# Kernel optimization log

Measured on AMD Instinct MI355X. Metric: run time of the kernel, lower is better.

## Reference

```python
import jax, jax.numpy as jnp
import numpy as np

B, N, DIM = 4, 2048, 512
H, DH, ORDER, TOPK = 8, 64, 3, 64
INNER = H * DH
SCALE = DH ** -0.5


def setup_inputs() -> dict:
    key = jax.random.key(0)
    ks = jax.random.split(key, 6)
    x = jax.random.normal(ks[0], (B, N, DIM), dtype=jnp.float32)
    Wqkv = jax.random.normal(ks[1], (DIM, 3 * INNER), dtype=jnp.float32) * (DIM ** -0.5)
    bqkv = jax.random.normal(ks[2], (3 * INNER,), dtype=jnp.float32) * 0.01
    Wout = jax.random.normal(ks[3], (INNER, DIM), dtype=jnp.float32) * (INNER ** -0.5)
    bout = jax.random.normal(ks[4], (DIM,), dtype=jnp.float32) * 0.01
    # init per reset_parameters for non-softmax/sigmoid/tanh act: ones/order
    alphas_raw = jnp.ones((ORDER, H), dtype=jnp.float32) / ORDER
    return {"x": x, "Wqkv": Wqkv, "bqkv": bqkv, "Wout": Wout, "bout": bout, "alphas_raw": alphas_raw}


def reference(x, Wqkv, bqkv, Wout, bout, alphas_raw):
    b, n, _ = x.shape
    qkv = x @ Wqkv + bqkv                                   # (b, n, 3*inner)
    q, k, v = jnp.split(qkv, 3, axis=-1)
    to_heads = lambda t: t.reshape(b, n, H, DH).transpose(0, 2, 1, 3)  # (b, h, n, d)
    q, k, v = to_heads(q), to_heads(k), to_heads(v)
    scores = jnp.einsum('bhnd,bhmd->bhnm', q, k) * SCALE    # (b, h, n, n)
    # top-k masking along last dim (keep ties with k-th value)
    top_val = jax.lax.top_k(scores, TOPK)[0][..., -1:]
    scores = jnp.where(scores < top_val, -jnp.inf, scores)
    attn = jax.nn.softmax(scores, axis=-1)
    # fp32 polynomial filter (monomial basis)
    attn32 = attn.astype(jnp.float32)
    v_curr = v.astype(jnp.float32)
    alphas = jax.nn.gelu(alphas_raw.astype(jnp.float32), approximate=False)  # (order, h)
    res = jnp.zeros_like(v_curr)
    for i in range(ORDER):
        v_curr = attn32 @ v_curr
        res = res + alphas[i].reshape(1, H, 1, 1) * v_curr
    out = res.astype(x.dtype).transpose(0, 2, 1, 3).reshape(b, n, INNER)
    return out @ Wout + bout
```

## Files before the change

### kernel.cpp

```cpp
#include <hip/hip_runtime.h>
#include <hip/hip_bf16.h>

#define SLOTS 80

typedef __bf16 bf16x8 __attribute__((ext_vector_type(8)));
typedef float  f32x4  __attribute__((ext_vector_type(4)));
typedef unsigned short u16x8 __attribute__((ext_vector_type(8)));

__global__ __launch_bounds__(256)
void sgemm_bias(const float* __restrict__ A, const float* __restrict__ Bm,
                const float* __restrict__ bias, float* __restrict__ C,
                int M, int N, int K)
{
    __shared__ float As[16][132];
    __shared__ float Bs[16][132];

    const int t  = threadIdx.x;
    const int tx = t & 15, ty = t >> 4;
    const int bm = blockIdx.y << 7, bn = blockIdx.x << 7;

    const int arow = t >> 2,  ak4 = (t & 3) << 2;
    const int bkr  = t >> 5,  bc4 = (t & 31) << 2;

    float4 pa[2], pb[2];
#pragma unroll
    for (int s = 0; s < 2; ++s) {
        pa[s] = *(const float4*)&A[(size_t)(bm + arow + (s << 6)) * K + ak4];
        pb[s] = *(const float4*)&Bm[(size_t)(bkr + (s << 3)) * N + bn + bc4];
    }

    float acc[8][8] = {};

    for (int k0 = 0; k0 < K; k0 += 16) {
        __syncthreads();
#pragma unroll
        for (int s = 0; s < 2; ++s) {
            const int ar = arow + (s << 6);
            As[ak4 + 0][ar] = pa[s].x;
            As[ak4 + 1][ar] = pa[s].y;
            As[ak4 + 2][ar] = pa[s].z;
            As[ak4 + 3][ar] = pa[s].w;
            *(float4*)&Bs[bkr + (s << 3)][bc4] = pb[s];
        }
        __syncthreads();
        if (k0 + 16 < K) {
#pragma unroll
            for (int s = 0; s < 2; ++s) {
                pa[s] = *(const float4*)&A[(size_t)(bm + arow + (s << 6)) * K + k0 + 16 + ak4];
                pb[s] = *(const float4*)&Bm[(size_t)(k0 + 16 + bkr + (s << 3)) * N + bn + bc4];
            }
        }
#pragma unroll
        for (int kk = 0; kk < 16; ++kk) {
            float4 a0 = *(const float4*)&As[kk][(ty << 3) + 0];
            float4 a1 = *(const float4*)&As[kk][(ty << 3) + 4];
            float4 b0 = *(const float4*)&Bs[kk][(tx << 2)];
            float4 b1 = *(const float4*)&Bs[kk][64 + (tx << 2)];
            float ar[8] = {a0.x, a0.y, a0.z, a0.w, a1.x, a1.y, a1.z, a1.w};
            float br[8] = {b0.x, b0.y, b0.z, b0.w, b1.x, b1.y, b1.z, b1.w};
#pragma unroll
            for (int i = 0; i < 8; ++i)
#pragma unroll
                for (int j = 0; j < 8; ++j)
                    acc[i][j] = fmaf(ar[i], br[j], acc[i][j]);
        }
    }

    float bb[8];
#pragma unroll
    for (int j = 0; j < 4; ++j) {
        bb[j]     = bias[bn + (tx << 2) + j];
        bb[j + 4] = bias[bn + 64 + (tx << 2) + j];
    }
#pragma unroll
    for (int i = 0; i < 8; ++i) {
        const size_t row = (size_t)(bm + (ty << 3) + i);
        float4 o0 = {acc[i][0] + bb[0], acc[i][1] + bb[1], acc[i][2] + bb[2], acc[i][3] + bb[3]};
        float4 o1 = {acc[i][4] + bb[4], acc[i][5] + bb[5], acc[i][6] + bb[6], acc[i][7] + bb[7]};
        *(float4*)&C[row * N + bn + (tx << 2)]      = o0;
        *(float4*)&C[row * N + bn + 64 + (tx << 2)] = o1;
    }
}

__global__ __launch_bounds__(256)
void qk_split(const float* __restrict__ qkv, unsigned short* __restrict__ qfrag,
              unsigned short* __restrict__ kfrag)
{
    const int gid = blockIdx.x * 256 + threadIdx.x;
    const int dg = gid & 7;
    const int h  = (gid >> 3) & 7;
    const int n  = (gid >> 6) & 2047;
    const int b  = gid >> 17;
    const int bh = (b << 3) + h;

    const size_t src = ((size_t)(b * 2048 + n)) * 1536 + (h << 6) + (dg << 3);

    const int tb = n >> 4;
    const int c  = n & 15;
    const int ks = dg >> 2;
    const int ln = c | ((dg & 3) << 4);
    const size_t base0 = ((((size_t)bh * 128 + tb) * 6 + ks) * 64 + ln) * 8;

#pragma unroll
    for (int qk = 0; qk < 2; ++qk) {
        const float4 x0 = *(const float4*)&qkv[src + (qk ? 512 : 0)];
        const float4 x1 = *(const float4*)&qkv[src + (qk ? 512 : 0) + 4];
        unsigned short* outp = qk ? kfrag : qfrag;
        const float xs[8] = {x0.x, x0.y, x0.z, x0.w, x1.x, x1.y, x1.z, x1.w};
        u16x8 vh, vm, vl;
#pragma unroll
        for (int j = 0; j < 8; ++j) {
            const float x = xs[j];
            __hip_bfloat16 h0 = __float2bfloat16(x);
            const float f0 = __bfloat162float(h0);
            const float r1 = x - f0;
            __hip_bfloat16 h1 = __float2bfloat16(r1);
            const float f1 = __bfloat162float(h1);
            const float r2 = r1 - f1;
            __hip_bfloat16 h2 = __float2bfloat16(r2);
            vh[j] = *(unsigned short*)&h0;
            vm[j] = *(unsigned short*)&h1;
            vl[j] = *(unsigned short*)&h2;
        }
        *(u16x8*)(outp + base0)        = vh;
        *(u16x8*)(outp + base0 + 1024) = vm;
        *(u16x8*)(outp + base0 + 2048) = vl;
    }
}

__global__ __launch_bounds__(512, 2)
void scores_topk(const unsigned short* __restrict__ qfrag,
                 const unsigned short* __restrict__ kfrag,
                 float* __restrict__ svals,
                 unsigned short* __restrict__ sidx, int* __restrict__ scnt)
{
    __shared__ float S[16][2052];

    const int t    = threadIdx.x;
    const int lane = t & 63;
    const int wid  = t >> 6;
    const int id   = blockIdx.x;
    const int bh   = ((id >> 10) << 3) | (id & 7);
    const int rowblk = (id >> 3) & 127;
    const int r0   = rowblk << 4;

    const bf16x8* qf = (const bf16x8*)qfrag
                     + (((size_t)bh * 128 + rowblk) * 6) * 64 + lane;
    bf16x8 afr[6];
#pragma unroll
    for (int f = 0; f < 6; ++f) afr[f] = qf[f * 64];

    const bf16x8* kf = (const bf16x8*)kfrag + ((size_t)bh * 128 * 6) * 64 + lane;

#define MCHAIN(ACC, B0, B1, B2, B3, B4, B5)                                    \
        ACC = __builtin_amdgcn_mfma_f32_16x16x32_bf16(afr[0], B0, ACC, 0, 0, 0); \
        ACC = __builtin_amdgcn_mfma_f32_16x16x32_bf16(afr[1], B1, ACC, 0, 0, 0); \
        ACC = __builtin_amdgcn_mfma_f32_16x16x32_bf16(afr[0], B2, ACC, 0, 0, 0); \
        ACC = __builtin_amdgcn_mfma_f32_16x16x32_bf16(afr[1], B3, ACC, 0, 0, 0); \
        ACC = __builtin_amdgcn_mfma_f32_16x16x32_bf16(afr[2], B0, ACC, 0, 0, 0); \
        ACC = __builtin_amdgcn_mfma_f32_16x16x32_bf16(afr[3], B1, ACC, 0, 0, 0); \
        ACC = __builtin_amdgcn_mfma_f32_16x16x32_bf16(afr[2], B2, ACC, 0, 0, 0); \
        ACC = __builtin_amdgcn_mfma_f32_16x16x32_bf16(afr[3], B3, ACC, 0, 0, 0); \
        ACC = __builtin_amdgcn_mfma_f32_16x16x32_bf16(afr[0], B4, ACC, 0, 0, 0); \
        ACC = __builtin_amdgcn_mfma_f32_16x16x32_bf16(afr[1], B5, ACC, 0, 0, 0); \
        ACC = __builtin_amdgcn_mfma_f32_16x16x32_bf16(afr[4], B0, ACC, 0, 0, 0); \
        ACC = __builtin_amdgcn_mfma_f32_16x16x32_bf16(afr[5], B1, ACC, 0, 0, 0);

#define STEP2(I)                                                               \
    {                                                                          \
        const int ct0 = (((I) << 1) << 3) + wid;                               \
        const int ct1 = ((((I) << 1) | 1) << 3) + wid;                         \
        const bf16x8* kb0 = kf + (size_t)ct0 * 384;                            \
        const bf16x8* kb1 = kf + (size_t)ct1 * 384;                            \
        bf16x8 b0 = kb0[0];   bf16x8 b1 = kb0[64];  bf16x8 b2 = kb0[128];      \
        bf16x8 b3 = kb0[192]; bf16x8 b4 = kb0[256]; bf16x8 b5 = kb0[320];      \
        bf16x8 c0 = kb1[0];   bf16x8 c1 = kb1[64];  bf16x8 c2 = kb1[128];      \
        bf16x8 c3 = kb1[192]; bf16x8 c4 = kb1[256]; bf16x8 c5 = kb1[320];      \
        f32x4 acc0 = {0.f, 0.f, 0.f, 0.f};                                     \
        MCHAIN(acc0, b0, b1, b2, b3, b4, b5)                                   \
        f32x4 acc1 = {0.f, 0.f, 0.f, 0.f};                                     \
        MCHAIN(acc1, c0, c1, c2, c3, c4, c5)                                   \
        const int rbase = (lane >> 4) << 2;                                    \
        const int col0  = (ct0 << 4) + (lane & 15);                            \
        const int col1  = (ct1 << 4) + (lane & 15);                            \
        S[rbase + 0][col0] = acc0[0] * 0.125f;                                 \
        S[rbase + 1][col0] = acc0[1] * 0.125f;                                 \
        S[rbase + 2][col0] = acc0[2] * 0.125f;                                 \
        S[rbase + 3][col0] = acc0[3] * 0.125f;                                 \
        S[rbase + 0][col1] = acc1[0] * 0.125f;                                 \
        S[rbase + 1][col1] = acc1[1] * 0.125f;                                 \
        S[rbase + 2][col1] = acc1[2] * 0.125f;                                 \
        S[rbase + 3][col1] = acc1[3] * 0.125f;                                 \
    }

    STEP2(0) STEP2(1) STEP2(2) STEP2(3)
    STEP2(4) STEP2(5) STEP2(6) STEP2(7)
#undef STEP2
#undef MCHAIN

    __syncthreads();

    const unsigned long long pre64 = (1ull << lane) - 1ull;

#define PHASEB(RQ)                                                             \
    {                                                                          \
        const int rr = (wid << 1) + (RQ);                                      \
        float    fv[32];                                                       \
        unsigned uv[32];                                                       \
        _Pragma("unroll")                                                      \
        for (int m = 0; m < 32; ++m) {                                         \
            const float x = S[rr][lane + (m << 6)];                            \
            fv[m] = x;                                                         \
            const unsigned bx = __float_as_uint(x);                            \
            uv[m] = bx ^ (unsigned)(((int)bx >> 31) | 0x80000000);             \
        }                                                                      \
        unsigned lo = 0;                                                       \
        _Pragma("unroll 1")                                                    \
        for (int bit = 31; bit >= 0; --bit) {                                  \
            const unsigned mid = lo | (1u << bit);                             \
            int c = 0;                                                         \
            _Pragma("unroll")                                                  \
            for (int m = 0; m < 32; ++m)                                       \
                c += __popcll(__ballot(uv[m] >= mid));                         \
            if (c >= 64) {                                                     \
                lo = mid;                                                      \
                if (c == 64) break;                                            \
            }                                                                  \
        }                                                                      \
        unsigned um = 0;                                                       \
        _Pragma("unroll")                                                      \
        for (int m = 0; m < 32; ++m) um = uv[m] > um ? uv[m] : um;             \
        _Pragma("unroll")                                                      \
        for (int off = 1; off < 64; off <<= 1) {                               \
            const unsigned o = (unsigned)__shfl_xor((int)um, off, 64);         \
            um = o > um ? o : um;                                              \
        }                                                                      \
        const unsigned mbm = (um & 0x80000000u) ? (um ^ 0x80000000u) : ~um;    \
        const float Mx = __uint_as_float(mbm);                                 \
        float zs = 0.f;                                                        \
        _Pragma("unroll")                                                      \
        for (int m = 0; m < 32; ++m) {                                         \
            const bool keep = uv[m] >= lo;                                     \
            const float ex = keep ? __expf(fv[m] - Mx) : 0.f;                  \
            fv[m] = ex;                                                        \
            zs += ex;                                                          \
        }                                                                      \
        _Pragma("unroll")                                                      \
        for (int off = 1; off < 64; off <<= 1) zs += __shfl_xor(zs, off, 64);  \
        const float zinv = 1.0f / zs;                                          \
        const size_t grow = (size_t)bh * 2048 + r0 + rr;                       \
        float* vd           = svals + grow * SLOTS;                            \
        unsigned short* idp = sidx  + grow * SLOTS;                            \
        int base = 0;                                                          \
        _Pragma("unroll")                                                      \
        for (int m = 0; m < 32; ++m) {                                         \
            const bool keep = uv[m] >= lo;                                     \
            unsigned long long ball = __ballot(keep);                          \
            if (keep) {                                                        \
                const int my = base + __popcll(ball & pre64);                  \
                if (my < SLOTS) {                                              \
                    vd[my]  = fv[m] * zinv;                                    \
                    idp[my] = (unsigned short)(lane + (m << 6));               \
                }                                                              \
            }                                                                  \
            base += __popcll(ball);                                            \
        }                                                                      \
        if (lane == 0) scnt[grow] = base < SLOTS ? base : SLOTS;               \
    }

    PHASEB(0)
    PHASEB(1)
#undef PHASEB
}

__global__ __launch_bounds__(256)
void spmm(const float* __restrict__ svals, const unsigned short* __restrict__ sidx,
          const int* __restrict__ scnt, const float* __restrict__ qkv,
          const float* __restrict__ vin, float* __restrict__ vout,
          float* __restrict__ res, const float* __restrict__ alphas_raw, int order)
{
    const int lane = threadIdx.x & 63;
    const int id   = blockIdx.x;
    const int bh   = ((id & 7) << 2) | (id >> 12);
    const int nblk = (id >> 3) & 511;
    const int n    = (nblk << 2) + (threadIdx.x >> 6);
    const int gr   = (bh << 11) + n;
    const int b    = bh >> 3,  h = bh & 7;

    const float* vb;
    int stride;
    if (order == 0) { vb = qkv + (size_t)b * 2048 * 1536 + 1024 + (h << 6); stride = 1536; }
    else            { vb = vin + ((size_t)bh << 17);                        stride = 64;   }

    const int cnt = scnt[gr];
    const float* va          = svals + (size_t)gr * SLOTS;
    const unsigned short* ia = sidx  + (size_t)gr * SLOTS;

    float acc = 0.f;
    int j = 0;
    for (; j + 8 <= cnt; j += 8) {
        float a0 = va[j],     a1 = va[j + 1], a2 = va[j + 2], a3 = va[j + 3];
        float a4 = va[j + 4], a5 = va[j + 5], a6 = va[j + 6], a7 = va[j + 7];
        int   i0 = ia[j],     i1 = ia[j + 1], i2 = ia[j + 2], i3 = ia[j + 3];
        int   i4 = ia[j + 4], i5 = ia[j + 5], i6 = ia[j + 6], i7 = ia[j + 7];
        acc += a0 * vb[(size_t)i0 * stride + lane];
        acc += a1 * vb[(size_t)i1 * stride + lane];
        acc += a2 * vb[(size_t)i2 * stride + lane];
        acc += a3 * vb[(size_t)i3 * stride + lane];
        acc += a4 * vb[(size_t)i4 * stride + lane];
        acc += a5 * vb[(size_t)i5 * stride + lane];
        acc += a6 * vb[(size_t)i6 * stride + lane];
        acc += a7 * vb[(size_t)i7 * stride + lane];
    }
    for (; j < cnt; ++j) acc += va[j] * vb[(size_t)ia[j] * stride + lane];

    if (order < 2) vout[((size_t)gr << 6) + lane] = acc;

    float ar    = alphas_raw[(order << 3) + h];
    float alpha = ar * 0.5f * (1.0f + erff(ar * 0.70710678f));
    size_t ro = ((size_t)b * 2048 + n) * 512 + (h << 6) + lane;
    float av  = alpha * acc;
    if (order == 0) res[ro] = av;
    else            res[ro] += av;
}

extern "C" void kernel_launch(void* const* d_in, const int* in_sizes, int n_in,
                              void* d_out, int out_size, void* d_ws, size_t ws_size,
                              hipStream_t stream)
{
    const float* x      = (const float*)d_in[0];
    const float* Wqkv   = (const float*)d_in[1];
    const float* bqkv   = (const float*)d_in[2];
    const float* Wout   = (const float*)d_in[3];
    const float* bout   = (const float*)d_in[4];
    const float* alphas = (const float*)d_in[5];
    float* out = (float*)d_out;

    char* ws = (char*)d_ws;
    float*          qkvb  = (float*)ws;
    float*          svals = (float*)(ws + 50331648);
    unsigned short* sidxp = (unsigned short*)(ws + 71303168);
    int*            scntp = (int*)(ws + 81788928);
    unsigned short* qfrag = (unsigned short*)(ws + 82051072);
    unsigned short* kfrag = (unsigned short*)(ws + 107216896);
    float*          v1    = (float*)(ws + 82051072);
    float*          v2    = (float*)(ws + 98828288);
    float*          resb  = (float*)(ws + 115605504);
    if (ws_size < 132382720) return;

    sgemm_bias<<<dim3(1536 / 128, 8192 / 128), 256, 0, stream>>>(
        x, Wqkv, bqkv, qkvb, 8192, 1536, 512);

    qk_split<<<2048, 256, 0, stream>>>(qkvb, qfrag, kfrag);

    scores_topk<<<4096, 512, 0, stream>>>(qfrag, kfrag, svals, sidxp, scntp);

    spmm<<<16384, 256, 0, stream>>>(svals, sidxp, scntp, qkvb, nullptr, v1, resb, alphas, 0);
    spmm<<<16384, 256, 0, stream>>>(svals, sidxp, scntp, qkvb, v1, v2, resb, alphas, 1);
    spmm<<<16384, 256, 0, stream>>>(svals, sidxp, scntp, qkvb, v2, nullptr, resb, alphas, 2);

    sgemm_bias<<<dim3(512 / 128, 8192 / 128), 256, 0, stream>>>(
        resb, Wout, bout, out, 8192, 512, 512);
}
```

Measured before the change: 974.3 us.

## Halve scores_topk LDS tile by splitting rows into two register-held phases

The score tile in shared memory shrinks from 16 to 8 rows. Each wave now writes only the first two of its four MFMA accumulator rows to LDS and keeps the other two in a 32-entry register array. The top-k/softmax phase runs on the first half, then the held rows are written back into LDS after a barrier and processed in a second pass. The aim is to fit two workgroups per CU instead of one, and the launch bound is raised to 4 blocks per CU. The cost is two extra barriers, less parallel MFMA issue, and a tighter register cap that, with the live register array plus fv/uv, may cause spills.

```diff
diff --git a/kernel.cpp b/kernel.cpp
--- a/kernel.cpp
+++ b/kernel.cpp
@@ -128,13 +128,13 @@
     }
 }
 
-__global__ __launch_bounds__(512, 2)
+__global__ __launch_bounds__(512, 4)
 void scores_topk(const unsigned short* __restrict__ qfrag,
                  const unsigned short* __restrict__ kfrag,
                  float* __restrict__ svals,
                  unsigned short* __restrict__ sidx, int* __restrict__ scnt)
 {
-    __shared__ float S[16][2052];
+    __shared__ float S[8][2052];
 
     const int t    = threadIdx.x;
     const int lane = t & 63;
@@ -152,64 +152,53 @@
 
     const bf16x8* kf = (const bf16x8*)kfrag + ((size_t)bh * 128 * 6) * 64 + lane;
 
-#define MCHAIN(ACC, B0, B1, B2, B3, B4, B5)                                    \
-        ACC = __builtin_amdgcn_mfma_f32_16x16x32_bf16(afr[0], B0, ACC, 0, 0, 0); \
-        ACC = __builtin_amdgcn_mfma_f32_16x16x32_bf16(afr[1], B1, ACC, 0, 0, 0); \
-        ACC = __builtin_amdgcn_mfma_f32_16x16x32_bf16(afr[0], B2, ACC, 0, 0, 0); \
-        ACC = __builtin_amdgcn_mfma_f32_16x16x32_bf16(afr[1], B3, ACC, 0, 0, 0); \
-        ACC = __builtin_amdgcn_mfma_f32_16x16x32_bf16(afr[2], B0, ACC, 0, 0, 0); \
-        ACC = __builtin_amdgcn_mfma_f32_16x16x32_bf16(afr[3], B1, ACC, 0, 0, 0); \
-        ACC = __builtin_amdgcn_mfma_f32_16x16x32_bf16(afr[2], B2, ACC, 0, 0, 0); \
-        ACC = __builtin_amdgcn_mfma_f32_16x16x32_bf16(afr[3], B3, ACC, 0, 0, 0); \
-        ACC = __builtin_amdgcn_mfma_f32_16x16x32_bf16(afr[0], B4, ACC, 0, 0, 0); \
-        ACC = __builtin_amdgcn_mfma_f32_16x16x32_bf16(afr[1], B5, ACC, 0, 0, 0); \
-        ACC = __builtin_amdgcn_mfma_f32_16x16x32_bf16(afr[4], B0, ACC, 0, 0, 0); \
-        ACC = __builtin_amdgcn_mfma_f32_16x16x32_bf16(afr[5], B1, ACC, 0, 0, 0);
-
-#define STEP2(I)                                                               \
+    const int slot0 = (lane >> 4) << 1;
+    float def[32];
+
+#define STEP(I)                                                                \
     {                                                                          \
-        const int ct0 = (((I) << 1) << 3) + wid;                               \
-        const int ct1 = ((((I) << 1) | 1) << 3) + wid;                         \
-        const bf16x8* kb0 = kf + (size_t)ct0 * 384;                            \
-        const bf16x8* kb1 = kf + (size_t)ct1 * 384;                            \
-        bf16x8 b0 = kb0[0];   bf16x8 b1 = kb0[64];  bf16x8 b2 = kb0[128];      \
-        bf16x8 b3 = kb0[192]; bf16x8 b4 = kb0[256]; bf16x8 b5 = kb0[320];      \
-        bf16x8 c0 = kb1[0];   bf16x8 c1 = kb1[64];  bf16x8 c2 = kb1[128];      \
-        bf16x8 c3 = kb1[192]; bf16x8 c4 = kb1[256]; bf16x8 c5 = kb1[320];      \
-        f32x4 acc0 = {0.f, 0.f, 0.f, 0.f};                                     \
-        MCHAIN(acc0, b0, b1, b2, b3, b4, b5)                                   \
-        f32x4 acc1 = {0.f, 0.f, 0.f, 0.f};                                     \
-        MCHAIN(acc1, c0, c1, c2, c3, c4, c5)                                   \
-        const int rbase = (lane >> 4) << 2;                                    \
-        const int col0  = (ct0 << 4) + (lane & 15);                            \
-        const int col1  = (ct1 << 4) + (lane & 15);                            \
-        S[rbase + 0][col0] = acc0[0] * 0.125f;                                 \
-        S[rbase + 1][col0] = acc0[1] * 0.125f;                                 \
-        S[rbase + 2][col0] = acc0[2] * 0.125f;                                 \
-        S[rbase + 3][col0] = acc0[3] * 0.125f;                                 \
-        S[rbase + 0][col1] = acc1[0] * 0.125f;                                 \
-        S[rbase + 1][col1] = acc1[1] * 0.125f;                                 \
-        S[rbase + 2][col1] = acc1[2] * 0.125f;                                 \
-        S[rbase + 3][col1] = acc1[3] * 0.125f;                                 \
-    }
-
-    STEP2(0) STEP2(1) STEP2(2) STEP2(3)
-    STEP2(4) STEP2(5) STEP2(6) STEP2(7)
-#undef STEP2
-#undef MCHAIN
+        const int ct = ((I) << 3) + wid;                                       \
+        const bf16x8* kb = kf + (size_t)ct * 384;                              \
+        bf16x8 b0 = kb[0];   bf16x8 b1 = kb[64];  bf16x8 b2 = kb[128];         \
+        bf16x8 b3 = kb[192]; bf16x8 b4 = kb[256]; bf16x8 b5 = kb[320];         \
+        f32x4 acc = {0.f, 0.f, 0.f, 0.f};                                      \
+        acc = __builtin_amdgcn_mfma_f32_16x16x32_bf16(afr[0], b0, acc, 0, 0, 0); \
+        acc = __builtin_amdgcn_mfma_f32_16x16x32_bf16(afr[1], b1, acc, 0, 0, 0); \
+        acc = __builtin_amdgcn_mfma_f32_16x16x32_bf16(afr[0], b2, acc, 0, 0, 0); \
+        acc = __builtin_amdgcn_mfma_f32_16x16x32_bf16(afr[1], b3, acc, 0, 0, 0); \
+        acc = __builtin_amdgcn_mfma_f32_16x16x32_bf16(afr[2], b0, acc, 0, 0, 0); \
+        acc = __builtin_amdgcn_mfma_f32_16x16x32_bf16(afr[3], b1, acc, 0, 0, 0); \
+        acc = __builtin_amdgcn_mfma_f32_16x16x32_bf16(afr[2], b2, acc, 0, 0, 0); \
+        acc = __builtin_amdgcn_mfma_f32_16x16x32_bf16(afr[3], b3, acc, 0, 0, 0); \
+        acc = __builtin_amdgcn_mfma_f32_16x16x32_bf16(afr[0], b4, acc, 0, 0, 0); \
+        acc = __builtin_amdgcn_mfma_f32_16x16x32_bf16(afr[1], b5, acc, 0, 0, 0); \
+        acc = __builtin_amdgcn_mfma_f32_16x16x32_bf16(afr[4], b0, acc, 0, 0, 0); \
+        acc = __builtin_amdgcn_mfma_f32_16x16x32_bf16(afr[5], b1, acc, 0, 0, 0); \
+        const int col = (ct << 4) + (lane & 15);                               \
+        S[slot0 + 0][col] = acc[0] * 0.125f;                                   \
+        S[slot0 + 1][col] = acc[1] * 0.125f;                                   \
+        def[2 * (I)]     = acc[2] * 0.125f;                                    \
+        def[2 * (I) + 1] = acc[3] * 0.125f;                                    \
+    }
+
+    STEP(0)  STEP(1)  STEP(2)  STEP(3)
+    STEP(4)  STEP(5)  STEP(6)  STEP(7)
+    STEP(8)  STEP(9)  STEP(10) STEP(11)
+    STEP(12) STEP(13) STEP(14) STEP(15)
+#undef STEP
 
     __syncthreads();
 
     const unsigned long long pre64 = (1ull << lane) - 1ull;
 
-#define PHASEB(RQ)                                                             \
+#define PHASEB(ROWOFF)                                                         \
     {                                                                          \
-        const int rr = (wid << 1) + (RQ);                                      \
+        const int rrow = (((wid >> 1) << 2) | (wid & 1)) + (ROWOFF);           \
         float    fv[32];                                                       \
         unsigned uv[32];                                                       \
         _Pragma("unroll")                                                      \
         for (int m = 0; m < 32; ++m) {                                         \
-            const float x = S[rr][lane + (m << 6)];                            \
+            const float x = S[wid][lane + (m << 6)];                           \
             fv[m] = x;                                                         \
             const unsigned bx = __float_as_uint(x);                            \
             uv[m] = bx ^ (unsigned)(((int)bx >> 31) | 0x80000000);             \
@@ -248,7 +237,7 @@
         _Pragma("unroll")                                                      \
         for (int off = 1; off < 64; off <<= 1) zs += __shfl_xor(zs, off, 64);  \
         const float zinv = 1.0f / zs;                                          \
-        const size_t grow = (size_t)bh * 2048 + r0 + rr;                       \
+        const size_t grow = (size_t)bh * 2048 + r0 + rrow;                     \
         float* vd           = svals + grow * SLOTS;                            \
         unsigned short* idp = sidx  + grow * SLOTS;                            \
         int base = 0;                                                          \
@@ -269,7 +258,18 @@
     }
 
     PHASEB(0)
-    PHASEB(1)
+
+    __syncthreads();
+
+#pragma unroll
+    for (int I = 0; I < 16; ++I) {
+        const int col = (((I << 3) + wid) << 4) + (lane & 15);
+        S[slot0 + 0][col] = def[2 * I];
+        S[slot0 + 1][col] = def[2 * I + 1];
+    }
+    __syncthreads();
+
+    PHASEB(2)
 #undef PHASEB
 }
 
```

New measurement: 804.1 us (median of 2 runs). 1.21x faster.
